# Kernel optimization log

Hardware: AMD Instinct MI355X
Metric: run time of the kernel (lower is better)

## Reference

```python
import jax, jax.numpy as jnp
import numpy as np

B, S, H, C = 8, 4096, 768, 64

def setup_inputs() -> dict:
    key = jax.random.key(0)
    ks = jax.random.split(key, 13)
    s_h = 1.0 / np.sqrt(H)
    s_c = 1.0 / np.sqrt(C)
    return {
        "hidden_states": jax.random.normal(ks[0], (B, S, H), jnp.float32),
        "attention_mask": jnp.ones((B, S), jnp.int32),
        # contrast_transform: Linear(H, C)
        "W_ct": jax.random.uniform(ks[1], (H, C), jnp.float32, -s_h, s_h),
        "b_ct": jax.random.uniform(ks[2], (C,), jnp.float32, -s_h, s_h),
        # conflict_detector: Linear(C, 1)
        "W_cd": jax.random.uniform(ks[3], (C, 1), jnp.float32, -s_c, s_c),
        "b_cd": jax.random.uniform(ks[4], (1,), jnp.float32, -s_c, s_c),
        # expectation_mlp: Linear(H,C) -> ReLU -> Linear(C,1)
        "W_e1": jax.random.uniform(ks[5], (H, C), jnp.float32, -s_h, s_h),
        "b_e1": jax.random.uniform(ks[6], (C,), jnp.float32, -s_h, s_h),
        "W_e2": jax.random.uniform(ks[7], (C, 1), jnp.float32, -s_c, s_c),
        "b_e2": jax.random.uniform(ks[8], (1,), jnp.float32, -s_c, s_c),
        # surprise query/key: Linear(H, C)
        "W_q": jax.random.uniform(ks[9], (H, C), jnp.float32, -s_h, s_h),
        "b_q": jax.random.uniform(ks[10], (C,), jnp.float32, -s_h, s_h),
        "W_k": jax.random.uniform(ks[11], (H, C), jnp.float32, -s_h, s_h),
        "b_k": jax.random.uniform(ks[12], (C,), jnp.float32, -s_h, s_h),
    }

def reference(hidden_states, attention_mask, W_ct, b_ct, W_cd, b_cd,
              W_e1, b_e1, W_e2, b_e2, W_q, b_q, W_k, b_k):
    # semantic conflict: sigmoid(Linear1(Linear(h)))  -> (B, S)
    compressed = hidden_states @ W_ct + b_ct                      # (B,S,C)
    semantic_conflict = jax.nn.sigmoid((compressed @ W_cd + b_cd)[..., 0])
    # expectation violation: sigmoid(MLP(h)) -> (B, S)
    h1 = jax.nn.relu(hidden_states @ W_e1 + b_e1)                 # (B,S,C)
    expectation_violation = jax.nn.sigmoid((h1 @ W_e2 + b_e2)[..., 0])
    # contextual surprise: mean over keys of softmax(QK^T / sqrt(C))
    Q = hidden_states @ W_q + b_q                                 # (B,S,C)
    K = hidden_states @ W_k + b_k                                 # (B,S,C)
    scores = jnp.einsum('bqc,bkc->bqk', Q, K) / jnp.sqrt(jnp.float32(Q.shape[-1]))
    contextual_surprise = jnp.mean(jax.nn.softmax(scores, axis=-1), axis=-1)  # (B,S)
    return semantic_conflict, expectation_violation, contextual_surprise
```

## Files before the change

kernel.cpp:

```cpp
#include <hip/hip_runtime.h>
#include <hip/hip_bf16.h>
#include <math.h>

typedef __bf16 bf16;
typedef __bf16 bf16x8 __attribute__((ext_vector_type(8)));
typedef float  f32x4  __attribute__((ext_vector_type(4)));

static constexpr int kTokens = 32768;
static constexpr int kH   = 768;
static constexpr int kC   = 64;
static constexpr int kNW  = 80;
static constexpr int kLDW = kH + 8;

__global__ void prep_kernel(const float* __restrict__ W_ct,
                            const float* __restrict__ b_ct,
                            const float* __restrict__ W_cd,
                            const float* __restrict__ b_cd,
                            const float* __restrict__ W_e1,
                            bf16* __restrict__ Wt,
                            float* __restrict__ bsc) {
    int gidx = blockIdx.x * blockDim.x + threadIdx.x;
    const int total = kNW * kH;
    if (gidx < total) {
        int n = gidx / kH;
        int k = gidx - n * kH;
        float v = 0.f;
        if (n < kC) {
            v = W_e1[k * kC + n];
        } else if (n == kC) {
            float s = 0.f;
            for (int c = 0; c < kC; ++c) s += W_ct[k * kC + c] * W_cd[c];
            v = s;
        }
        Wt[gidx] = (bf16)v;
    } else if (gidx == total) {
        float s = b_cd[0];
        for (int c = 0; c < kC; ++c) s += b_ct[c] * W_cd[c];
        bsc[0] = s;
    }
}

__global__ __launch_bounds__(512, 2) void incong_main(
    const float* __restrict__ hs,
    const bf16*  __restrict__ Wt,
    const float* __restrict__ bsc_p,
    const float* __restrict__ b_e1,
    const float* __restrict__ W_e2,
    const float* __restrict__ b_e2,
    float* __restrict__ out)
{
    __shared__ bf16 lds_w[kNW][kLDW];

    const int tid  = threadIdx.x;
    const int lane = tid & 63;
    const int wv   = tid >> 6;
    const int r16  = lane & 15;
    const int kg   = lane >> 4;

    constexpr int kChunks = kNW * (kH / 8);
    for (int c = tid; c < kChunks; c += 512) {
        int row = c / (kH / 8);
        int col = (c - row * (kH / 8)) * 8;
        *reinterpret_cast<bf16x8*>(&lds_w[row][col]) =
            *reinterpret_cast<const bf16x8*>(&Wt[(size_t)row * kH + col]);
    }
    __syncthreads();

    const int tok0 = (blockIdx.x * 8 + wv) * 16;

    f32x4 acc[5];
    #pragma unroll
    for (int n = 0; n < 5; ++n) acc[n] = (f32x4){0.f, 0.f, 0.f, 0.f};

    const float* ap = hs + (size_t)(tok0 + r16) * kH + kg * 8;
    const bf16* lp = &lds_w[r16][kg * 8];

    #pragma unroll 8
    for (int ks = 0; ks < kH; ks += 32) {
        const float4 a0 = *reinterpret_cast<const float4*>(ap + ks);
        const float4 a1 = *reinterpret_cast<const float4*>(ap + ks + 4);
        bf16x8 af;
        af[0] = (bf16)a0.x; af[1] = (bf16)a0.y; af[2] = (bf16)a0.z; af[3] = (bf16)a0.w;
        af[4] = (bf16)a1.x; af[5] = (bf16)a1.y; af[6] = (bf16)a1.z; af[7] = (bf16)a1.w;
        #pragma unroll
        for (int n = 0; n < 5; ++n) {
            const bf16x8 bfr = *reinterpret_cast<const bf16x8*>(
                lp + (size_t)(n * 16) * kLDW + ks);
            acc[n] = __builtin_amdgcn_mfma_f32_16x16x32_bf16(af, bfr, acc[n], 0, 0, 0);
        }
    }

    float part[4] = {0.f, 0.f, 0.f, 0.f};
    #pragma unroll
    for (int n = 0; n < 4; ++n) {
        const int cidx = n * 16 + r16;
        const float be = b_e1[cidx];
        const float we = W_e2[cidx];
        #pragma unroll
        for (int r = 0; r < 4; ++r)
            part[r] += fmaxf(acc[n][r] + be, 0.f) * we;
    }
    #pragma unroll
    for (int m = 1; m < 16; m <<= 1) {
        #pragma unroll
        for (int r = 0; r < 4; ++r) part[r] += __shfl_xor(part[r], m);
    }
    if (r16 == 0) {
        const float bsc = bsc_p[0];
        const float be2 = b_e2[0];
        #pragma unroll
        for (int r = 0; r < 4; ++r) {
            const int tok = tok0 + kg * 4 + r;
            const float sc = acc[4][r] + bsc;
            out[tok]               = 1.f / (1.f + __expf(-sc));
            out[kTokens + tok]     = 1.f / (1.f + __expf(-(part[r] + be2)));
            out[2 * kTokens + tok] = 1.f / 4096.f;
        }
    }
}

extern "C" void kernel_launch(void* const* d_in, const int* in_sizes, int n_in,
                              void* d_out, int out_size, void* d_ws, size_t ws_size,
                              hipStream_t stream) {
    const float* hs   = (const float*)d_in[0];
    const float* W_ct = (const float*)d_in[2];
    const float* b_ct = (const float*)d_in[3];
    const float* W_cd = (const float*)d_in[4];
    const float* b_cd = (const float*)d_in[5];
    const float* W_e1 = (const float*)d_in[6];
    const float* b_e1 = (const float*)d_in[7];
    const float* W_e2 = (const float*)d_in[8];
    const float* b_e2 = (const float*)d_in[9];

    bf16*  Wt  = (bf16*)d_ws;
    float* bsc = (float*)((char*)d_ws + (size_t)kNW * kH * sizeof(bf16));

    const int prep_total = kNW * kH + 1;
    prep_kernel<<<(prep_total + 255) / 256, 256, 0, stream>>>(
        W_ct, b_ct, W_cd, b_cd, W_e1, Wt, bsc);

    incong_main<<<kTokens / (16 * 8), 512, 0, stream>>>(
        hs, Wt, bsc, b_e1, W_e2, b_e2, (float*)d_out);
}
```

Baseline: 30.45 us.

## Prefetch hidden-state tiles ahead of MFMA loop and trim weight staging

```diff
diff --git a/kernel.cpp b/kernel.cpp
--- a/kernel.cpp
+++ b/kernel.cpp
@@ -9,7 +9,7 @@
 static constexpr int kTokens = 32768;
 static constexpr int kH   = 768;
 static constexpr int kC   = 64;
-static constexpr int kNW  = 80;
+static constexpr int kNWr = 65;
 static constexpr int kLDW = kH + 8;
 
 __global__ void prep_kernel(const float* __restrict__ W_ct,
@@ -20,20 +20,17 @@
                             bf16* __restrict__ Wt,
                             float* __restrict__ bsc) {
     int gidx = blockIdx.x * blockDim.x + threadIdx.x;
-    const int total = kNW * kH;
-    if (gidx < total) {
-        int n = gidx / kH;
-        int k = gidx - n * kH;
-        float v = 0.f;
-        if (n < kC) {
-            v = W_e1[k * kC + n];
-        } else if (n == kC) {
-            float s = 0.f;
-            for (int c = 0; c < kC; ++c) s += W_ct[k * kC + c] * W_cd[c];
-            v = s;
-        }
-        Wt[gidx] = (bf16)v;
-    } else if (gidx == total) {
+    if (gidx < kH * kC) {
+        int k = gidx >> 6;
+        int n = gidx & 63;
+        Wt[(size_t)n * kH + k] = (bf16)W_e1[gidx];
+    } else if (gidx < kH * kC + kH) {
+        int k = gidx - kH * kC;
+        float s = 0.f;
+        #pragma unroll 8
+        for (int c = 0; c < kC; ++c) s += W_ct[k * kC + c] * W_cd[c];
+        Wt[(size_t)kC * kH + k] = (bf16)s;
+    } else if (gidx == kH * kC + kH) {
         float s = b_cd[0];
         for (int c = 0; c < kC; ++c) s += b_ct[c] * W_cd[c];
         bsc[0] = s;
@@ -49,15 +46,26 @@
     const float* __restrict__ b_e2,
     float* __restrict__ out)
 {
-    __shared__ bf16 lds_w[kNW][kLDW];
-
+    __shared__ bf16 lds_w[80][kLDW];
     const int tid  = threadIdx.x;
     const int lane = tid & 63;
     const int wv   = tid >> 6;
     const int r16  = lane & 15;
     const int kg   = lane >> 4;
 
-    constexpr int kChunks = kNW * (kH / 8);
+    const int tok0 = (blockIdx.x * 8 + wv) * 16;
+    const float* ap = hs + (size_t)(tok0 + r16) * kH + kg * 8;
+
+    float4 a00 = *reinterpret_cast<const float4*>(ap + 0);
+    float4 a01 = *reinterpret_cast<const float4*>(ap + 4);
+    float4 a10 = *reinterpret_cast<const float4*>(ap + 32);
+    float4 a11 = *reinterpret_cast<const float4*>(ap + 36);
+    float4 c00 = *reinterpret_cast<const float4*>(ap + 64);
+    float4 c01 = *reinterpret_cast<const float4*>(ap + 68);
+    float4 c10 = *reinterpret_cast<const float4*>(ap + 96);
+    float4 c11 = *reinterpret_cast<const float4*>(ap + 100);
+
+    constexpr int kChunks = kNWr * (kH / 8);
     for (int c = tid; c < kChunks; c += 512) {
         int row = c / (kH / 8);
         int col = (c - row * (kH / 8)) * 8;
@@ -66,28 +74,41 @@
     }
     __syncthreads();
 
-    const int tok0 = (blockIdx.x * 8 + wv) * 16;
-
     f32x4 acc[5];
     #pragma unroll
     for (int n = 0; n < 5; ++n) acc[n] = (f32x4){0.f, 0.f, 0.f, 0.f};
 
-    const float* ap = hs + (size_t)(tok0 + r16) * kH + kg * 8;
     const bf16* lp = &lds_w[r16][kg * 8];
 
-    #pragma unroll 8
-    for (int ks = 0; ks < kH; ks += 32) {
-        const float4 a0 = *reinterpret_cast<const float4*>(ap + ks);
-        const float4 a1 = *reinterpret_cast<const float4*>(ap + ks + 4);
+    #pragma unroll
+    for (int ks = 0; ks < kH; ks += 64) {
+        float4 n00, n01, n10, n11;
+        if (ks < kH - 128) {
+            n00 = *reinterpret_cast<const float4*>(ap + ks + 128);
+            n01 = *reinterpret_cast<const float4*>(ap + ks + 132);
+            n10 = *reinterpret_cast<const float4*>(ap + ks + 160);
+            n11 = *reinterpret_cast<const float4*>(ap + ks + 164);
+        }
         bf16x8 af;
-        af[0] = (bf16)a0.x; af[1] = (bf16)a0.y; af[2] = (bf16)a0.z; af[3] = (bf16)a0.w;
-        af[4] = (bf16)a1.x; af[5] = (bf16)a1.y; af[6] = (bf16)a1.z; af[7] = (bf16)a1.w;
+        af[0] = (bf16)a00.x; af[1] = (bf16)a00.y; af[2] = (bf16)a00.z; af[3] = (bf16)a00.w;
+        af[4] = (bf16)a01.x; af[5] = (bf16)a01.y; af[6] = (bf16)a01.z; af[7] = (bf16)a01.w;
         #pragma unroll
         for (int n = 0; n < 5; ++n) {
             const bf16x8 bfr = *reinterpret_cast<const bf16x8*>(
                 lp + (size_t)(n * 16) * kLDW + ks);
             acc[n] = __builtin_amdgcn_mfma_f32_16x16x32_bf16(af, bfr, acc[n], 0, 0, 0);
         }
+        bf16x8 ag;
+        ag[0] = (bf16)a10.x; ag[1] = (bf16)a10.y; ag[2] = (bf16)a10.z; ag[3] = (bf16)a10.w;
+        ag[4] = (bf16)a11.x; ag[5] = (bf16)a11.y; ag[6] = (bf16)a11.z; ag[7] = (bf16)a11.w;
+        #pragma unroll
+        for (int n = 0; n < 5; ++n) {
+            const bf16x8 bfr = *reinterpret_cast<const bf16x8*>(
+                lp + (size_t)(n * 16) * kLDW + ks + 32);
+            acc[n] = __builtin_amdgcn_mfma_f32_16x16x32_bf16(ag, bfr, acc[n], 0, 0, 0);
+        }
+        a00 = c00; a01 = c01; a10 = c10; a11 = c11;
+        if (ks < kH - 128) { c00 = n00; c01 = n01; c10 = n10; c11 = n11; }
     }
 
     float part[4] = {0.f, 0.f, 0.f, 0.f};
@@ -133,9 +154,9 @@
     const float* b_e2 = (const float*)d_in[9];
 
     bf16*  Wt  = (bf16*)d_ws;
-    float* bsc = (float*)((char*)d_ws + (size_t)kNW * kH * sizeof(bf16));
+    float* bsc = (float*)((char*)d_ws + (size_t)80 * kH * sizeof(bf16));
 
-    const int prep_total = kNW * kH + 1;
+    const int prep_total = kH * kC + kH + 1;
     prep_kernel<<<(prep_total + 255) / 256, 256, 0, stream>>>(
         W_ct, b_ct, W_cd, b_cd, W_e1, Wt, bsc);
 
```

Result: no change. 30.58 us (+0.4%).

## Stage weights in two K-halves to shrink LDS and coalesce prep transpose

Applied to the files above, without the earlier changes.

```diff
diff --git a/kernel.cpp b/kernel.cpp
--- a/kernel.cpp
+++ b/kernel.cpp
@@ -9,38 +9,72 @@
 static constexpr int kTokens = 32768;
 static constexpr int kH   = 768;
 static constexpr int kC   = 64;
-static constexpr int kNW  = 80;
-static constexpr int kLDW = kH + 8;
+static constexpr int kKH  = 384;
+static constexpr int kLDW = kKH + 8;
 
-__global__ void prep_kernel(const float* __restrict__ W_ct,
-                            const float* __restrict__ b_ct,
-                            const float* __restrict__ W_cd,
-                            const float* __restrict__ b_cd,
-                            const float* __restrict__ W_e1,
-                            bf16* __restrict__ Wt,
-                            float* __restrict__ bsc) {
-    int gidx = blockIdx.x * blockDim.x + threadIdx.x;
-    const int total = kNW * kH;
-    if (gidx < total) {
-        int n = gidx / kH;
-        int k = gidx - n * kH;
-        float v = 0.f;
-        if (n < kC) {
-            v = W_e1[k * kC + n];
-        } else if (n == kC) {
+__global__ __launch_bounds__(256) void prep_kernel(
+    const float* __restrict__ W_ct, const float* __restrict__ b_ct,
+    const float* __restrict__ W_cd, const float* __restrict__ b_cd,
+    const float* __restrict__ W_e1, bf16* __restrict__ Wt,
+    float* __restrict__ bsc) {
+    __shared__ float t[64][65];
+    const int tid = threadIdx.x;
+    const int b   = blockIdx.x;
+    if (b < 12) {
+        const int k0 = b * 64;
+        #pragma unroll
+        for (int i = 0; i < 16; ++i) {
+            int idx = tid + i * 256;
+            int k = idx >> 6, n = idx & 63;
+            t[k][n] = W_e1[(size_t)(k0 + k) * kC + n];
+        }
+        __syncthreads();
+        #pragma unroll
+        for (int i = 0; i < 16; ++i) {
+            int idx = tid + i * 256;
+            int n = idx >> 6, k = idx & 63;
+            Wt[(size_t)n * kH + k0 + k] = (bf16)t[k][n];
+        }
+    } else if (b < 24) {
+        const int k0 = (b - 12) * 64;
+        #pragma unroll
+        for (int i = 0; i < 16; ++i) {
+            int idx = tid + i * 256;
+            int k = idx >> 6, c = idx & 63;
+            t[k][c] = W_ct[(size_t)(k0 + k) * kC + c];
+        }
+        __syncthreads();
+        if (tid < 64) {
             float s = 0.f;
-            for (int c = 0; c < kC; ++c) s += W_ct[k * kC + c] * W_cd[c];
-            v = s;
+            #pragma unroll
+            for (int c = 0; c < kC; ++c) s += t[tid][c] * W_cd[c];
+            Wt[(size_t)kC * kH + k0 + tid] = (bf16)s;
         }
-        Wt[gidx] = (bf16)v;
-    } else if (gidx == total) {
-        float s = b_cd[0];
-        for (int c = 0; c < kC; ++c) s += b_ct[c] * W_cd[c];
-        bsc[0] = s;
+    } else {
+        if (tid < 64) {
+            float v = b_ct[tid] * W_cd[tid];
+            #pragma unroll
+            for (int m = 1; m < 64; m <<= 1) v += __shfl_xor(v, m);
+            if (tid == 0) bsc[0] = v + b_cd[0];
+        }
     }
 }
 
-__global__ __launch_bounds__(512, 2) void incong_main(
+__device__ __forceinline__ void stage_half(const bf16* __restrict__ Wt, int h,
+                                           bf16 (*lds_w)[kLDW], int tid) {
+    #pragma unroll
+    for (int j = 0; j < 7; ++j) {
+        int c = tid + j * 512;
+        if (j < 6 || c < 3120) {
+            int row = c / 48;
+            int col = (c - row * 48) * 8;
+            *reinterpret_cast<bf16x8*>(&lds_w[row][col]) =
+                *reinterpret_cast<const bf16x8*>(&Wt[(size_t)row * kH + h * kKH + col]);
+        }
+    }
+}
+
+__global__ __launch_bounds__(512, 4) void incong_main(
     const float* __restrict__ hs,
     const bf16*  __restrict__ Wt,
     const float* __restrict__ bsc_p,
@@ -49,7 +83,7 @@
     const float* __restrict__ b_e2,
     float* __restrict__ out)
 {
-    __shared__ bf16 lds_w[kNW][kLDW];
+    __shared__ bf16 lds_w[65][kLDW];
 
     const int tid  = threadIdx.x;
     const int lane = tid & 63;
@@ -57,36 +91,55 @@
     const int r16  = lane & 15;
     const int kg   = lane >> 4;
 
-    constexpr int kChunks = kNW * (kH / 8);
-    for (int c = tid; c < kChunks; c += 512) {
-        int row = c / (kH / 8);
-        int col = (c - row * (kH / 8)) * 8;
-        *reinterpret_cast<bf16x8*>(&lds_w[row][col]) =
-            *reinterpret_cast<const bf16x8*>(&Wt[(size_t)row * kH + col]);
-    }
-    __syncthreads();
-
     const int tok0 = (blockIdx.x * 8 + wv) * 16;
+    const float* ap = hs + (size_t)(tok0 + r16) * kH + kg * 8;
 
     f32x4 acc[5];
     #pragma unroll
     for (int n = 0; n < 5; ++n) acc[n] = (f32x4){0.f, 0.f, 0.f, 0.f};
 
-    const float* ap = hs + (size_t)(tok0 + r16) * kH + kg * 8;
-    const bf16* lp = &lds_w[r16][kg * 8];
+    const bf16* lp  = &lds_w[r16][kg * 8];
+    const bf16* lp4 = &lds_w[64][kg * 8];
 
-    #pragma unroll 8
-    for (int ks = 0; ks < kH; ks += 32) {
-        const float4 a0 = *reinterpret_cast<const float4*>(ap + ks);
-        const float4 a1 = *reinterpret_cast<const float4*>(ap + ks + 4);
-        bf16x8 af;
-        af[0] = (bf16)a0.x; af[1] = (bf16)a0.y; af[2] = (bf16)a0.z; af[3] = (bf16)a0.w;
-        af[4] = (bf16)a1.x; af[5] = (bf16)a1.y; af[6] = (bf16)a1.z; af[7] = (bf16)a1.w;
+    #pragma unroll
+    for (int h = 0; h < 2; ++h) {
+        if (h) __syncthreads();
+        stage_half(Wt, h, lds_w, tid);
+        __syncthreads();
+
+        const float* aph = ap + h * kKH;
         #pragma unroll
-        for (int n = 0; n < 5; ++n) {
-            const bf16x8 bfr = *reinterpret_cast<const bf16x8*>(
-                lp + (size_t)(n * 16) * kLDW + ks);
-            acc[n] = __builtin_amdgcn_mfma_f32_16x16x32_bf16(af, bfr, acc[n], 0, 0, 0);
+        for (int ks = 0; ks < kKH; ks += 64) {
+            const float4 a0 = *reinterpret_cast<const float4*>(aph + ks);
+            const float4 a1 = *reinterpret_cast<const float4*>(aph + ks + 4);
+            const float4 a2 = *reinterpret_cast<const float4*>(aph + ks + 32);
+            const float4 a3 = *reinterpret_cast<const float4*>(aph + ks + 36);
+            bf16x8 af;
+            af[0] = (bf16)a0.x; af[1] = (bf16)a0.y; af[2] = (bf16)a0.z; af[3] = (bf16)a0.w;
+            af[4] = (bf16)a1.x; af[5] = (bf16)a1.y; af[6] = (bf16)a1.z; af[7] = (bf16)a1.w;
+            #pragma unroll
+            for (int n = 0; n < 4; ++n) {
+                const bf16x8 bfr = *reinterpret_cast<const bf16x8*>(
+                    lp + (size_t)(n * 16) * kLDW + ks);
+                acc[n] = __builtin_amdgcn_mfma_f32_16x16x32_bf16(af, bfr, acc[n], 0, 0, 0);
+            }
+            {
+                const bf16x8 b4 = *reinterpret_cast<const bf16x8*>(lp4 + ks);
+                acc[4] = __builtin_amdgcn_mfma_f32_16x16x32_bf16(af, b4, acc[4], 0, 0, 0);
+            }
+            bf16x8 ag;
+            ag[0] = (bf16)a2.x; ag[1] = (bf16)a2.y; ag[2] = (bf16)a2.z; ag[3] = (bf16)a2.w;
+            ag[4] = (bf16)a3.x; ag[5] = (bf16)a3.y; ag[6] = (bf16)a3.z; ag[7] = (bf16)a3.w;
+            #pragma unroll
+            for (int n = 0; n < 4; ++n) {
+                const bf16x8 bfr = *reinterpret_cast<const bf16x8*>(
+                    lp + (size_t)(n * 16) * kLDW + ks + 32);
+                acc[n] = __builtin_amdgcn_mfma_f32_16x16x32_bf16(ag, bfr, acc[n], 0, 0, 0);
+            }
+            {
+                const bf16x8 b4 = *reinterpret_cast<const bf16x8*>(lp4 + ks + 32);
+                acc[4] = __builtin_amdgcn_mfma_f32_16x16x32_bf16(ag, b4, acc[4], 0, 0, 0);
+            }
         }
     }
 
@@ -133,11 +186,9 @@
     const float* b_e2 = (const float*)d_in[9];
 
     bf16*  Wt  = (bf16*)d_ws;
-    float* bsc = (float*)((char*)d_ws + (size_t)kNW * kH * sizeof(bf16));
+    float* bsc = (float*)((char*)d_ws + (size_t)80 * kH * sizeof(bf16));
 
-    const int prep_total = kNW * kH + 1;
-    prep_kernel<<<(prep_total + 255) / 256, 256, 0, stream>>>(
-        W_ct, b_ct, W_cd, b_cd, W_e1, Wt, bsc);
+    prep_kernel<<<25, 256, 0, stream>>>(W_ct, b_ct, W_cd, b_cd, W_e1, Wt, bsc);
 
     incong_main<<<kTokens / (16 * 8), 512, 0, stream>>>(
         hs, Wt, bsc, b_e1, W_e2, b_e2, (float*)d_out);
```

Result: faster. 28.81 us (-5.4%).
